# Performance work log

Measured on AMD Instinct MI355X. Metric: run time of the kernel, lower is better.

## Reference

```python
import jax, jax.numpy as jnp
import numpy as np

MODEL_DIM = 1024
NUM_HEADS = 16
HEAD_DIM = MODEL_DIM // NUM_HEADS
B, T = 4, 2048


def setup_inputs() -> dict:
    key = jax.random.key(0)
    ks = jax.random.split(key, 11)
    s = 1.0 / np.sqrt(MODEL_DIM)  # torch Linear default-ish init scale
    def lin(kw, kb):
        W = jax.random.uniform(kw, (MODEL_DIM, MODEL_DIM), jnp.float32, -s, s)
        b = jax.random.uniform(kb, (MODEL_DIM,), jnp.float32, -s, s)
        return W, b
    Wq, bq = lin(ks[0], ks[1])
    Wk, bk = lin(ks[2], ks[3])
    Wv, bv = lin(ks[4], ks[5])
    Wo, bo = lin(ks[6], ks[7])
    query = jax.random.normal(ks[8], (B, T, MODEL_DIM), jnp.float32)
    key_t = jax.random.normal(ks[9], (B, T, MODEL_DIM), jnp.float32)
    value = jax.random.normal(ks[10], (B, T, MODEL_DIM), jnp.float32)
    return {"query": query, "key": key_t, "value": value,
            "Wq": Wq, "bq": bq, "Wk": Wk, "bk": bk,
            "Wv": Wv, "bv": bv, "Wo": Wo, "bo": bo}


def reference(query, key, value, Wq, bq, Wk, bk, Wv, bv, Wo, bo):
    b, tq, d = query.shape
    tk = key.shape[-2]
    h, hd = NUM_HEADS, HEAD_DIM
    # projections; split last dim into heads (torch split/cat == reshape to [b,t,h,hd])
    q = (query @ Wq.T + bq).reshape(b, tq, h, hd)
    k = (key @ Wk.T + bk).reshape(b, tk, h, hd)
    v = (value @ Wv.T + bv).reshape(b, tk, h, hd)
    score = jnp.einsum('bqhd,bkhd->bhqk', q, k) / np.sqrt(hd).astype(np.float32)
    causal = jnp.tril(jnp.ones((tq, tk), dtype=bool))  # mask=True path
    score = jnp.where(causal, score, -jnp.inf)
    probs = jax.nn.softmax(score, axis=-1)
    out = jnp.einsum('bhqk,bkhd->bqhd', probs, v).reshape(b, tq, d)
    return out @ Wo.T + bo
```

## Files before the change

kernel.cpp:

```cpp
#include <hip/hip_runtime.h>
#include <stdint.h>

#define T_SEQ 2048
#define NB    4
#define NH    16
#define DH    64
#define DM    1024
#define MTOT  (NB * T_SEQ)

typedef __attribute__((ext_vector_type(8)))  short  short8;
typedef __attribute__((ext_vector_type(8)))  __bf16 bf16x8;
typedef __attribute__((ext_vector_type(4)))  float  f32x4;
typedef __attribute__((ext_vector_type(16))) float  f32x16;
typedef __attribute__((ext_vector_type(4)))  unsigned short ushort4v;
typedef __attribute__((ext_vector_type(4)))  unsigned int   uint4v;
typedef unsigned short ushort;
typedef unsigned long long u64;

__device__ __forceinline__ ushort f2bf(float x) {
    unsigned int u = __builtin_bit_cast(unsigned int, x);
    u += 0x7FFFu + ((u >> 16) & 1u);
    return (ushort)(u >> 16);
}

__device__ __forceinline__ unsigned cvtpk(float lo, float hi) {
    unsigned r;
    asm("v_cvt_pk_bf16_f32 %0, %1, %2" : "=v"(r) : "v"(lo), "v"(hi));
    return r;
}

__device__ __forceinline__ f32x4 mfma16(short8 a, short8 b, f32x4 c) {
    return __builtin_amdgcn_mfma_f32_16x16x32_bf16(
        __builtin_bit_cast(bf16x8, a), __builtin_bit_cast(bf16x8, b), c, 0, 0, 0);
}
__device__ __forceinline__ f32x16 mfma32(short8 a, short8 b, f32x16 c) {
    return __builtin_amdgcn_mfma_f32_32x32x16_bf16(
        __builtin_bit_cast(bf16x8, a), __builtin_bit_cast(bf16x8, b), c, 0, 0, 0);
}

#define GLOBAL_AS(p) ((const __attribute__((address_space(1))) void*)(p))
#define LDS_AS(p)    ((__attribute__((address_space(3))) void*)(p))

__global__ void cvt4_kernel(const float* __restrict__ s0, const float* __restrict__ s1,
                            const float* __restrict__ s2, const float* __restrict__ s3,
                            ushort* __restrict__ dst) {
    int i = blockIdx.x * 256 + threadIdx.x;
    int which = i >> 18;
    int loc   = i & 262143;
    const float* s = which == 0 ? s0 : which == 1 ? s1 : which == 2 ? s2 : s3;
    f32x4 v = ((const f32x4*)s)[loc];
    ushort4v r;
    r[0] = f2bf(v[0]); r[1] = f2bf(v[1]); r[2] = f2bf(v[2]); r[3] = f2bf(v[3]);
    ((ushort4v*)dst)[i] = r;
}

template <int MODE>
__global__ __launch_bounds__(256, 2)
void gemm_kernel(const void* __restrict__ Xv, const ushort* __restrict__ Wb,
                 const float* __restrict__ bias, void* __restrict__ outv, float scale)
{
    __shared__ __align__(16) ushort sA[128 * 64];
    __shared__ __align__(16) ushort sB[128 * 64];

    const int tid  = threadIdx.x;
    const int lane = tid & 63;
    const int w    = tid >> 6;
    const int wr   = (w >> 1) * 64;
    const int wc   = (w & 1) * 64;
    const int bm   = (blockIdx.x & 63) * 128;
    const int bn   = (blockIdx.x >> 6) * 128;
    const int lr   = lane & 15;
    const int lk   = lane >> 4;

    f32x4 acc[4][4] = {};

    for (int kt = 0; kt < DM; kt += 64) {
        __syncthreads();
        if constexpr (MODE == 0 || MODE == 2) {
            const float* X = (const float*)Xv;
            #pragma unroll
            for (int i = 0; i < 4; ++i) {
                int ofs  = i * 4096 + w * 1024 + lane * 16;
                int row  = ofs >> 7;
                int colB = ofs & 127;
                const float* src = X + (size_t)(bm + row) * DM + kt + (colB >> 1);
                f32x4 v0 = *(const f32x4*)(src);
                f32x4 v1 = *(const f32x4*)(src + 4);
                short8 pk;
                pk[0] = (short)f2bf(v0[0]); pk[1] = (short)f2bf(v0[1]);
                pk[2] = (short)f2bf(v0[2]); pk[3] = (short)f2bf(v0[3]);
                pk[4] = (short)f2bf(v1[0]); pk[5] = (short)f2bf(v1[1]);
                pk[6] = (short)f2bf(v1[2]); pk[7] = (short)f2bf(v1[3]);
                *(short8*)((char*)sA + row * 128 + (colB ^ ((row & 7) << 4))) = pk;
            }
        } else {
            const ushort* X = (const ushort*)Xv;
            #pragma unroll
            for (int i = 0; i < 4; ++i) {
                int ofs  = i * 4096 + w * 1024 + lane * 16;
                int row  = ofs >> 7;
                int colB = (ofs & 127) ^ ((row & 7) << 4);
                const char* src = (const char*)X + ((size_t)(bm + row) * DM + kt) * 2 + colB;
                char* dst = (char*)sA + i * 4096 + w * 1024;
                __builtin_amdgcn_global_load_lds(GLOBAL_AS(src), LDS_AS(dst), 16, 0, 0);
            }
        }
        #pragma unroll
        for (int i = 0; i < 4; ++i) {
            int ofs  = i * 4096 + w * 1024 + lane * 16;
            int row  = ofs >> 7;
            int colB = (ofs & 127) ^ ((row & 7) << 4);
            const char* src = (const char*)Wb + ((size_t)(bn + row) * DM + kt) * 2 + colB;
            char* dst = (char*)sB + i * 4096 + w * 1024;
            __builtin_amdgcn_global_load_lds(GLOBAL_AS(src), LDS_AS(dst), 16, 0, 0);
        }
        __syncthreads();

        #pragma unroll
        for (int kk = 0; kk < 2; ++kk) {
            short8 af[4], bfr[4];
            #pragma unroll
            for (int m = 0; m < 4; ++m) {
                int row = wr + m * 16 + lr;
                int cB  = (kk * 64 + lk * 16) ^ ((row & 7) << 4);
                af[m] = *(const short8*)((const char*)sA + row * 128 + cB);
            }
            #pragma unroll
            for (int n = 0; n < 4; ++n) {
                int row = wc + n * 16 + lr;
                int cB  = (kk * 64 + lk * 16) ^ ((row & 7) << 4);
                bfr[n] = *(const short8*)((const char*)sB + row * 128 + cB);
            }
            #pragma unroll
            for (int m = 0; m < 4; ++m)
                #pragma unroll
                for (int n = 0; n < 4; ++n)
                    acc[m][n] = mfma16(af[m], bfr[n], acc[m][n]);
        }
    }

    #pragma unroll
    for (int m = 0; m < 4; ++m) {
        #pragma unroll
        for (int n = 0; n < 4; ++n) {
            int col   = bn + wc + n * 16 + lr;
            float bv  = bias[col];
            if constexpr (MODE == 2) {
                int row0 = bm + wr + m * 16 + lk * 4;
                int b = row0 >> 11, t0 = row0 & (T_SEQ - 1);
                int h = col >> 6,  d = col & 63;
                int t0p = (t0 & ~12) | ((t0 & 4) << 1) | ((t0 & 8) >> 1);
                u64 pk = 0;
                #pragma unroll
                for (int j = 0; j < 4; ++j)
                    pk |= (u64)f2bf(acc[m][n][j] + bv) << (16 * j);
                *(u64*)((ushort*)outv + ((size_t)((b * NH + h) * DH + d)) * T_SEQ + t0p) = pk;
            } else {
                #pragma unroll
                for (int j = 0; j < 4; ++j) {
                    int row   = bm + wr + m * 16 + lk * 4 + j;
                    float val = (acc[m][n][j] + bv) * scale;
                    if constexpr (MODE == 0) {
                        int b = row >> 11, t = row & (T_SEQ - 1);
                        int h = col >> 6,  d = col & 63;
                        ((ushort*)outv)[((size_t)((b * NH + h) * T_SEQ + t)) * DH + d] = f2bf(val);
                    } else {
                        ((float*)outv)[(size_t)row * DM + col] = val;
                    }
                }
            }
        }
    }
}

__global__ __launch_bounds__(256)
void attn_kernel(const ushort* __restrict__ Q, const ushort* __restrict__ K,
                 const ushort* __restrict__ Vt, ushort* __restrict__ O)
{
    __shared__ __align__(16) ushort sK[2][64 * 64];
    __shared__ __align__(16) ushort sV[2][64 * 64];

    const int tid  = threadIdx.x;
    const int lane = tid & 63;
    const int w    = tid >> 6;
    const int l31  = lane & 31;
    const int hi   = lane >> 5;
    const int bh   = blockIdx.x & 63;
    const int qt   = 15 - (blockIdx.x >> 6);
    const int b    = bh >> 4, h = bh & 15;

    const ushort* Qbh = Q + (size_t)bh * T_SEQ * DH;
    const char*   Kc  = (const char*)(K  + (size_t)bh * T_SEQ * DH);
    const char*   Vc  = (const char*)(Vt + (size_t)bh * DH * T_SEQ);

    const int q0w   = qt * 128 + w * 32;
    const int kvmax = 2 * qt + 1;

    const int scolB = (tid & 7) * 16;

    auto STAGE = [&](int kv, int buf) {
        #pragma unroll
        for (int i = 0; i < 2; ++i) {
            int row = i * 32 + (tid >> 3);
            int cB  = scolB ^ ((row & 7) << 4);
            __builtin_amdgcn_global_load_lds(
                GLOBAL_AS(Kc + (size_t)(kv * 64 + row) * 128 + cB),
                LDS_AS((char*)&sK[buf][0] + i * 4096 + tid * 16), 16, 0, 0);
        }
        #pragma unroll
        for (int i = 0; i < 2; ++i) {
            int row = i * 32 + (tid >> 3);
            int cB  = scolB ^ ((row & 7) << 4);
            __builtin_amdgcn_global_load_lds(
                GLOBAL_AS(Vc + (size_t)row * (T_SEQ * 2) + kv * 128 + cB),
                LDS_AS((char*)&sV[buf][0] + i * 4096 + tid * 16), 16, 0, 0);
        }
    };

    short8 qf[4];
    #pragma unroll
    for (int dc = 0; dc < 4; ++dc)
        qf[dc] = *(const short8*)(Qbh + (size_t)(q0w + l31) * DH + dc * 16 + hi * 8);

    f32x16 o0 = {}, o1 = {};
    float mrow = -1e30f, lsum = 0.f;

    STAGE(0, 0);

    for (int kv = 0; kv <= kvmax; ++kv) {
        const int cur = kv & 1;
        __syncthreads();
        if (kv < kvmax) STAGE(kv + 1, cur ^ 1);
        if (kv * 64 > q0w + 31) continue;

        const char* sk = (const char*)&sK[cur][0];
        const char* sv = (const char*)&sV[cur][0];

        f32x16 s0 = {}, s1 = {};
        __builtin_amdgcn_s_setprio(1);
        #pragma unroll
        for (int dc = 0; dc < 4; ++dc) {
            int cB  = dc * 32 + hi * 16;
            int swz = (l31 & 7) << 4;
            short8 kf0 = *(const short8*)(sk + l31 * 128 + (cB ^ swz));
            short8 kf1 = *(const short8*)(sk + (32 + l31) * 128 + (cB ^ swz));
            s0 = mfma32(kf0, qf[dc], s0);
            s1 = mfma32(kf1, qf[dc], s1);
        }
        __builtin_amdgcn_s_setprio(0);

        if (kv * 64 + 63 > q0w) {
            int q = q0w + l31;
            #pragma unroll
            for (int r = 0; r < 16; ++r) {
                int kp = kv * 64 + (r & 3) + 8 * (r >> 2) + 4 * hi;
                if (kp > q)      s0[r] = -1e30f;
                if (kp + 32 > q) s1[r] = -1e30f;
            }
        }

        float t16[16];
        #pragma unroll
        for (int r = 0; r < 16; ++r) t16[r] = fmaxf(s0[r], s1[r]);
        #pragma unroll
        for (int r = 0; r < 8; ++r)  t16[r] = fmaxf(t16[r], t16[r + 8]);
        #pragma unroll
        for (int r = 0; r < 4; ++r)  t16[r] = fmaxf(t16[r], t16[r + 4]);
        float pm = fmaxf(fmaxf(t16[0], t16[1]), fmaxf(t16[2], t16[3]));
        pm = fmaxf(pm, __shfl_xor(pm, 32));

        if (__any(pm > mrow + 8.f)) {
            float mn = fmaxf(mrow, pm);
            float al = __builtin_amdgcn_exp2f(mrow - mn);
            mrow = mn;
            lsum *= al;
            #pragma unroll
            for (int r = 0; r < 16; ++r) {
                float aq = __shfl(al, (r & 3) + 8 * (r >> 2) + 4 * hi);
                o0[r] *= aq;
                o1[r] *= aq;
            }
        }

        float rs = 0.f;
        #pragma unroll
        for (int r = 0; r < 16; ++r) { s0[r] = __builtin_amdgcn_exp2f(s0[r] - mrow); rs += s0[r]; }
        #pragma unroll
        for (int r = 0; r < 16; ++r) { s1[r] = __builtin_amdgcn_exp2f(s1[r] - mrow); rs += s1[r]; }
        lsum += rs;

        short8 pa[4];
        #pragma unroll
        for (int seg = 0; seg < 4; ++seg) {
            const f32x16& sp = (seg < 2) ? s0 : s1;
            const int r0 = (seg & 1) * 8;
            uint4v pw;
            pw[0] = cvtpk(sp[r0 + 0], sp[r0 + 1]);
            pw[1] = cvtpk(sp[r0 + 2], sp[r0 + 3]);
            pw[2] = cvtpk(sp[r0 + 4], sp[r0 + 5]);
            pw[3] = cvtpk(sp[r0 + 6], sp[r0 + 7]);
            pa[seg] = __builtin_bit_cast(short8, pw);
        }

        __builtin_amdgcn_s_setprio(1);
        #pragma unroll
        for (int seg = 0; seg < 4; ++seg) {
            int cB = seg * 32 + hi * 16;
            {
                int d = l31;
                short8 vf = *(const short8*)(sv + d * 128 + (cB ^ ((d & 7) << 4)));
                o0 = mfma32(pa[seg], vf, o0);
            }
            {
                int d = 32 + l31;
                short8 vf = *(const short8*)(sv + d * 128 + (cB ^ ((d & 7) << 4)));
                o1 = mfma32(pa[seg], vf, o1);
            }
        }
        __builtin_amdgcn_s_setprio(0);
    }

    lsum += __shfl_xor(lsum, 32);
    float rl = 1.0f / lsum;
    #pragma unroll
    for (int r = 0; r < 16; ++r) {
        int   ql = (r & 3) + 8 * (r >> 2) + 4 * hi;
        float rq = __shfl(rl, ql);
        int   t  = q0w + ql;
        size_t base = ((size_t)(b * T_SEQ) + t) * DM + h * DH;
        O[base + l31]      = f2bf(o0[r] * rq);
        O[base + 32 + l31] = f2bf(o1[r] * rq);
    }
}

extern "C" void kernel_launch(void* const* d_in, const int* in_sizes, int n_in,
                              void* d_out, int out_size, void* d_ws, size_t ws_size,
                              hipStream_t stream)
{
    const float* query = (const float*)d_in[0];
    const float* key_t = (const float*)d_in[1];
    const float* value = (const float*)d_in[2];
    const float* Wq = (const float*)d_in[3];
    const float* bq = (const float*)d_in[4];
    const float* Wk = (const float*)d_in[5];
    const float* bk = (const float*)d_in[6];
    const float* Wv = (const float*)d_in[7];
    const float* bv = (const float*)d_in[8];
    const float* Wo = (const float*)d_in[9];
    const float* bo = (const float*)d_in[10];
    float* out = (float*)d_out;

    char* ws = (char*)d_ws;
    const size_t WSZ = (size_t)DM * DM * 2;
    const size_t PSZ = (size_t)MTOT * DM * 2;
    ushort* Wq_b = (ushort*)(ws);
    ushort* Wk_b = (ushort*)(ws + WSZ);
    ushort* Wv_b = (ushort*)(ws + 2 * WSZ);
    ushort* Wo_b = (ushort*)(ws + 3 * WSZ);
    ushort* Qp   = (ushort*)(ws + 4 * WSZ);
    ushort* Kp   = (ushort*)(ws + 4 * WSZ + PSZ);
    ushort* Vt   = (ushort*)(ws + 4 * WSZ + 2 * PSZ);
    ushort* AO   = (ushort*)(ws + 4 * WSZ + 3 * PSZ);

    cvt4_kernel<<<4096, 256, 0, stream>>>(Wq, Wk, Wv, Wo, Wq_b);

    gemm_kernel<0><<<512, 256, 0, stream>>>(query, Wq_b, bq, Qp, 0.18033688011112042f);
    gemm_kernel<0><<<512, 256, 0, stream>>>(key_t, Wk_b, bk, Kp, 1.0f);
    gemm_kernel<2><<<512, 256, 0, stream>>>(value, Wv_b, bv, Vt, 1.0f);

    attn_kernel<<<64 * 16, 256, 0, stream>>>(Qp, Kp, Vt, AO);

    gemm_kernel<1><<<512, 256, 0, stream>>>(AO, Wo_b, bo, out, 1.0f);
}
```

Baseline: 183.2 us.

## Merge QKV projections, double-buffer GEMMs, pair causal tiles in attention

```diff
diff --git a/kernel.cpp b/kernel.cpp
--- a/kernel.cpp
+++ b/kernel.cpp
@@ -54,13 +54,148 @@
     ((ushort4v*)dst)[i] = r;
 }
 
-template <int MODE>
 __global__ __launch_bounds__(256, 2)
-void gemm_kernel(const void* __restrict__ Xv, const ushort* __restrict__ Wb,
-                 const float* __restrict__ bias, void* __restrict__ outv, float scale)
+void proj_gemm(const float* __restrict__ Xq, const float* __restrict__ Xk,
+               const float* __restrict__ Xv, const ushort* __restrict__ Wall,
+               const float* __restrict__ bq, const float* __restrict__ bk,
+               const float* __restrict__ bv, ushort* __restrict__ P0,
+               ushort* __restrict__ Vt, float qscale)
 {
-    __shared__ __align__(16) ushort sA[128 * 64];
-    __shared__ __align__(16) ushort sB[128 * 64];
+    __shared__ __align__(16) ushort sA[2][128 * 64];
+    __shared__ __align__(16) ushort sB[2][128 * 64];
+
+    const int which = blockIdx.x >> 9;
+    const int inner = blockIdx.x & 511;
+    const float* X     = which == 0 ? Xq : which == 1 ? Xk : Xv;
+    const ushort* Wb   = Wall + (size_t)which * DM * DM;
+    const float* bias  = which == 0 ? bq : which == 1 ? bk : bv;
+
+    const int tid  = threadIdx.x;
+    const int lane = tid & 63;
+    const int w    = tid >> 6;
+    const int wr   = (w >> 1) * 64;
+    const int wc   = (w & 1) * 64;
+    const int bm   = (inner & 63) * 128;
+    const int bn   = (inner >> 6) * 128;
+    const int lr   = lane & 15;
+    const int lk   = lane >> 4;
+
+    const int ofs0 = w * 1024 + lane * 16;
+
+    f32x4 areg[8];
+    auto LOAD_A = [&](int kt) {
+        #pragma unroll
+        for (int i = 0; i < 4; ++i) {
+            int ofs  = i * 4096 + ofs0;
+            int row  = ofs >> 7;
+            int colB = ofs & 127;
+            const float* src = X + (size_t)(bm + row) * DM + kt + (colB >> 1);
+            areg[2 * i]     = *(const f32x4*)(src);
+            areg[2 * i + 1] = *(const f32x4*)(src + 4);
+        }
+    };
+    auto WRITE_A = [&](int buf) {
+        #pragma unroll
+        for (int i = 0; i < 4; ++i) {
+            int ofs  = i * 4096 + ofs0;
+            int row  = ofs >> 7;
+            int colB = ofs & 127;
+            f32x4 v0 = areg[2 * i], v1 = areg[2 * i + 1];
+            bf16x8 pk;
+            pk[0] = (__bf16)v0[0]; pk[1] = (__bf16)v0[1];
+            pk[2] = (__bf16)v0[2]; pk[3] = (__bf16)v0[3];
+            pk[4] = (__bf16)v1[0]; pk[5] = (__bf16)v1[1];
+            pk[6] = (__bf16)v1[2]; pk[7] = (__bf16)v1[3];
+            *(bf16x8*)((char*)&sA[buf][0] + row * 128 + (colB ^ ((row & 7) << 4))) = pk;
+        }
+    };
+    auto STAGE_B = [&](int kt, int buf) {
+        #pragma unroll
+        for (int i = 0; i < 4; ++i) {
+            int ofs  = i * 4096 + ofs0;
+            int row  = ofs >> 7;
+            int colB = (ofs & 127) ^ ((row & 7) << 4);
+            __builtin_amdgcn_global_load_lds(
+                GLOBAL_AS((const char*)Wb + ((size_t)(bn + row) * DM + kt) * 2 + colB),
+                LDS_AS((char*)&sB[buf][0] + i * 4096 + ofs0), 16, 0, 0);
+        }
+    };
+
+    f32x4 acc[4][4] = {};
+
+    LOAD_A(0);
+    STAGE_B(0, 0);
+    WRITE_A(0);
+
+    for (int t = 0; t < 16; ++t) {
+        const int cur = t & 1;
+        __syncthreads();
+        if (t < 15) {
+            LOAD_A((t + 1) * 64);
+            STAGE_B((t + 1) * 64, cur ^ 1);
+        }
+        #pragma unroll
+        for (int kk = 0; kk < 2; ++kk) {
+            short8 af[4], bfr[4];
+            #pragma unroll
+            for (int m = 0; m < 4; ++m) {
+                int row = wr + m * 16 + lr;
+                int cB  = (kk * 64 + lk * 16) ^ ((row & 7) << 4);
+                af[m] = *(const short8*)((const char*)&sA[cur][0] + row * 128 + cB);
+            }
+            #pragma unroll
+            for (int n = 0; n < 4; ++n) {
+                int row = wc + n * 16 + lr;
+                int cB  = (kk * 64 + lk * 16) ^ ((row & 7) << 4);
+                bfr[n] = *(const short8*)((const char*)&sB[cur][0] + row * 128 + cB);
+            }
+            #pragma unroll
+            for (int m = 0; m < 4; ++m)
+                #pragma unroll
+                for (int n = 0; n < 4; ++n)
+                    acc[m][n] = mfma16(af[m], bfr[n], acc[m][n]);
+        }
+        if (t < 15) WRITE_A(cur ^ 1);
+    }
+
+    const float scale = (which == 0) ? qscale : 1.0f;
+    #pragma unroll
+    for (int m = 0; m < 4; ++m) {
+        #pragma unroll
+        for (int n = 0; n < 4; ++n) {
+            int col  = bn + wc + n * 16 + lr;
+            float bv = bias[col];
+            if (which == 2) {
+                int row0 = bm + wr + m * 16 + lk * 4;
+                int b = row0 >> 11, t0 = row0 & (T_SEQ - 1);
+                int h = col >> 6,  d = col & 63;
+                int t0p = (t0 & ~12) | ((t0 & 4) << 1) | ((t0 & 8) >> 1);
+                u64 pk = 0;
+                #pragma unroll
+                for (int j = 0; j < 4; ++j)
+                    pk |= (u64)f2bf(acc[m][n][j] + bv) << (16 * j);
+                *(u64*)(Vt + ((size_t)((b * NH + h) * DH + d)) * T_SEQ + t0p) = pk;
+            } else {
+                ushort* outp = P0 + (size_t)which * MTOT * DM;
+                #pragma unroll
+                for (int j = 0; j < 4; ++j) {
+                    int row   = bm + wr + m * 16 + lk * 4 + j;
+                    float val = (acc[m][n][j] + bv) * scale;
+                    int b = row >> 11, t = row & (T_SEQ - 1);
+                    int h = col >> 6,  d = col & 63;
+                    outp[((size_t)((b * NH + h) * T_SEQ + t)) * DH + d] = f2bf(val);
+                }
+            }
+        }
+    }
+}
+
+__global__ __launch_bounds__(256, 2)
+void out_gemm(const ushort* __restrict__ X, const ushort* __restrict__ Wb,
+              const float* __restrict__ bias, float* __restrict__ out)
+{
+    __shared__ __align__(16) ushort sA[2][128 * 64];
+    __shared__ __align__(16) ushort sB[2][128 * 64];
 
     const int tid  = threadIdx.x;
     const int lane = tid & 63;
@@ -71,51 +206,31 @@
     const int bn   = (blockIdx.x >> 6) * 128;
     const int lr   = lane & 15;
     const int lk   = lane >> 4;
-
-    f32x4 acc[4][4] = {};
-
-    for (int kt = 0; kt < DM; kt += 64) {
-        __syncthreads();
-        if constexpr (MODE == 0 || MODE == 2) {
-            const float* X = (const float*)Xv;
-            #pragma unroll
-            for (int i = 0; i < 4; ++i) {
-                int ofs  = i * 4096 + w * 1024 + lane * 16;
-                int row  = ofs >> 7;
-                int colB = ofs & 127;
-                const float* src = X + (size_t)(bm + row) * DM + kt + (colB >> 1);
-                f32x4 v0 = *(const f32x4*)(src);
-                f32x4 v1 = *(const f32x4*)(src + 4);
-                short8 pk;
-                pk[0] = (short)f2bf(v0[0]); pk[1] = (short)f2bf(v0[1]);
-                pk[2] = (short)f2bf(v0[2]); pk[3] = (short)f2bf(v0[3]);
-                pk[4] = (short)f2bf(v1[0]); pk[5] = (short)f2bf(v1[1]);
-                pk[6] = (short)f2bf(v1[2]); pk[7] = (short)f2bf(v1[3]);
-                *(short8*)((char*)sA + row * 128 + (colB ^ ((row & 7) << 4))) = pk;
-            }
-        } else {
-            const ushort* X = (const ushort*)Xv;
-            #pragma unroll
-            for (int i = 0; i < 4; ++i) {
-                int ofs  = i * 4096 + w * 1024 + lane * 16;
-                int row  = ofs >> 7;
-                int colB = (ofs & 127) ^ ((row & 7) << 4);
-                const char* src = (const char*)X + ((size_t)(bm + row) * DM + kt) * 2 + colB;
-                char* dst = (char*)sA + i * 4096 + w * 1024;
-                __builtin_amdgcn_global_load_lds(GLOBAL_AS(src), LDS_AS(dst), 16, 0, 0);
-            }
-        }
+    const int ofs0 = w * 1024 + lane * 16;
+
+    auto STAGE = [&](const ushort* src0, ushort (*dst)[128 * 64], int kt, int buf) {
         #pragma unroll
         for (int i = 0; i < 4; ++i) {
-            int ofs  = i * 4096 + w * 1024 + lane * 16;
+            int ofs  = i * 4096 + ofs0;
             int row  = ofs >> 7;
             int colB = (ofs & 127) ^ ((row & 7) << 4);
-            const char* src = (const char*)Wb + ((size_t)(bn + row) * DM + kt) * 2 + colB;
-            char* dst = (char*)sB + i * 4096 + w * 1024;
-            __builtin_amdgcn_global_load_lds(GLOBAL_AS(src), LDS_AS(dst), 16, 0, 0);
-        }
+            __builtin_amdgcn_global_load_lds(
+                GLOBAL_AS((const char*)src0 + ((size_t)row * DM + kt) * 2 + colB),
+                LDS_AS((char*)&dst[buf][0] + i * 4096 + ofs0), 16, 0, 0);
+        }
+    };
+
+    f32x4 acc[4][4] = {};
+    STAGE(X + (size_t)bm * DM, sA, 0, 0);
+    STAGE(Wb + (size_t)bn * DM, sB, 0, 0);
+
+    for (int t = 0; t < 16; ++t) {
+        const int cur = t & 1;
         __syncthreads();
-
+        if (t < 15) {
+            STAGE(X + (size_t)bm * DM, sA, (t + 1) * 64, cur ^ 1);
+            STAGE(Wb + (size_t)bn * DM, sB, (t + 1) * 64, cur ^ 1);
+        }
         #pragma unroll
         for (int kk = 0; kk < 2; ++kk) {
             short8 af[4], bfr[4];
@@ -123,13 +238,13 @@
             for (int m = 0; m < 4; ++m) {
                 int row = wr + m * 16 + lr;
                 int cB  = (kk * 64 + lk * 16) ^ ((row & 7) << 4);
-                af[m] = *(const short8*)((const char*)sA + row * 128 + cB);
+                af[m] = *(const short8*)((const char*)&sA[cur][0] + row * 128 + cB);
             }
             #pragma unroll
             for (int n = 0; n < 4; ++n) {
                 int row = wc + n * 16 + lr;
                 int cB  = (kk * 64 + lk * 16) ^ ((row & 7) << 4);
-                bfr[n] = *(const short8*)((const char*)sB + row * 128 + cB);
+                bfr[n] = *(const short8*)((const char*)&sB[cur][0] + row * 128 + cB);
             }
             #pragma unroll
             for (int m = 0; m < 4; ++m)
@@ -143,31 +258,12 @@
     for (int m = 0; m < 4; ++m) {
         #pragma unroll
         for (int n = 0; n < 4; ++n) {
-            int col   = bn + wc + n * 16 + lr;
-            float bv  = bias[col];
-            if constexpr (MODE == 2) {
-                int row0 = bm + wr + m * 16 + lk * 4;
-                int b = row0 >> 11, t0 = row0 & (T_SEQ - 1);
-                int h = col >> 6,  d = col & 63;
-                int t0p = (t0 & ~12) | ((t0 & 4) << 1) | ((t0 & 8) >> 1);
-                u64 pk = 0;
-                #pragma unroll
-                for (int j = 0; j < 4; ++j)
-                    pk |= (u64)f2bf(acc[m][n][j] + bv) << (16 * j);
-                *(u64*)((ushort*)outv + ((size_t)((b * NH + h) * DH + d)) * T_SEQ + t0p) = pk;
-            } else {
-                #pragma unroll
-                for (int j = 0; j < 4; ++j) {
-                    int row   = bm + wr + m * 16 + lk * 4 + j;
-                    float val = (acc[m][n][j] + bv) * scale;
-                    if constexpr (MODE == 0) {
-                        int b = row >> 11, t = row & (T_SEQ - 1);
-                        int h = col >> 6,  d = col & 63;
-                        ((ushort*)outv)[((size_t)((b * NH + h) * T_SEQ + t)) * DH + d] = f2bf(val);
-                    } else {
-                        ((float*)outv)[(size_t)row * DM + col] = val;
-                    }
-                }
+            int col  = bn + wc + n * 16 + lr;
+            float bv = bias[col];
+            #pragma unroll
+            for (int j = 0; j < 4; ++j) {
+                int row = bm + wr + m * 16 + lk * 4 + j;
+                out[(size_t)row * DM + col] = acc[m][n][j] + bv;
             }
         }
     }
@@ -185,23 +281,25 @@
     const int w    = tid >> 6;
     const int l31  = lane & 31;
     const int hi   = lane >> 5;
-    const int bh   = blockIdx.x & 63;
-    const int qt   = 15 - (blockIdx.x >> 6);
-    const int b    = bh >> 4, h = bh & 15;
+
+    const int B   = blockIdx.x;
+    const int xcd = B & 7;
+    const int j   = B >> 3;
+    const int bh  = ((j >> 3) << 3) | xcd;
+    const int p   = j & 7;
+    const int b   = bh >> 4, h = bh & 15;
 
     const ushort* Qbh = Q + (size_t)bh * T_SEQ * DH;
     const char*   Kc  = (const char*)(K  + (size_t)bh * T_SEQ * DH);
     const char*   Vc  = (const char*)(Vt + (size_t)bh * DH * T_SEQ);
 
-    const int q0w   = qt * 128 + w * 32;
-    const int kvmax = 2 * qt + 1;
-
     const int scolB = (tid & 7) * 16;
+    const int srow  = tid >> 3;
 
     auto STAGE = [&](int kv, int buf) {
         #pragma unroll
         for (int i = 0; i < 2; ++i) {
-            int row = i * 32 + (tid >> 3);
+            int row = i * 32 + srow;
             int cB  = scolB ^ ((row & 7) << 4);
             __builtin_amdgcn_global_load_lds(
                 GLOBAL_AS(Kc + (size_t)(kv * 64 + row) * 128 + cB),
@@ -209,7 +307,7 @@
         }
         #pragma unroll
         for (int i = 0; i < 2; ++i) {
-            int row = i * 32 + (tid >> 3);
+            int row = i * 32 + srow;
             int cB  = scolB ^ ((row & 7) << 4);
             __builtin_amdgcn_global_load_lds(
                 GLOBAL_AS(Vc + (size_t)row * (T_SEQ * 2) + kv * 128 + cB),
@@ -217,119 +315,125 @@
         }
     };
 
-    short8 qf[4];
-    #pragma unroll
-    for (int dc = 0; dc < 4; ++dc)
-        qf[dc] = *(const short8*)(Qbh + (size_t)(q0w + l31) * DH + dc * 16 + hi * 8);
-
-    f32x16 o0 = {}, o1 = {};
-    float mrow = -1e30f, lsum = 0.f;
-
-    STAGE(0, 0);
-
-    for (int kv = 0; kv <= kvmax; ++kv) {
-        const int cur = kv & 1;
-        __syncthreads();
-        if (kv < kvmax) STAGE(kv + 1, cur ^ 1);
-        if (kv * 64 > q0w + 31) continue;
-
-        const char* sk = (const char*)&sK[cur][0];
-        const char* sv = (const char*)&sV[cur][0];
-
-        f32x16 s0 = {}, s1 = {};
-        __builtin_amdgcn_s_setprio(1);
-        #pragma unroll
-        for (int dc = 0; dc < 4; ++dc) {
-            int cB  = dc * 32 + hi * 16;
-            int swz = (l31 & 7) << 4;
-            short8 kf0 = *(const short8*)(sk + l31 * 128 + (cB ^ swz));
-            short8 kf1 = *(const short8*)(sk + (32 + l31) * 128 + (cB ^ swz));
-            s0 = mfma32(kf0, qf[dc], s0);
-            s1 = mfma32(kf1, qf[dc], s1);
-        }
-        __builtin_amdgcn_s_setprio(0);
-
-        if (kv * 64 + 63 > q0w) {
-            int q = q0w + l31;
-            #pragma unroll
-            for (int r = 0; r < 16; ++r) {
-                int kp = kv * 64 + (r & 3) + 8 * (r >> 2) + 4 * hi;
-                if (kp > q)      s0[r] = -1e30f;
-                if (kp + 32 > q) s1[r] = -1e30f;
-            }
-        }
-
-        float t16[16];
-        #pragma unroll
-        for (int r = 0; r < 16; ++r) t16[r] = fmaxf(s0[r], s1[r]);
-        #pragma unroll
-        for (int r = 0; r < 8; ++r)  t16[r] = fmaxf(t16[r], t16[r + 8]);
-        #pragma unroll
-        for (int r = 0; r < 4; ++r)  t16[r] = fmaxf(t16[r], t16[r + 4]);
-        float pm = fmaxf(fmaxf(t16[0], t16[1]), fmaxf(t16[2], t16[3]));
-        pm = fmaxf(pm, __shfl_xor(pm, 32));
-
-        if (__any(pm > mrow + 8.f)) {
-            float mn = fmaxf(mrow, pm);
-            float al = __builtin_amdgcn_exp2f(mrow - mn);
-            mrow = mn;
-            lsum *= al;
-            #pragma unroll
-            for (int r = 0; r < 16; ++r) {
-                float aq = __shfl(al, (r & 3) + 8 * (r >> 2) + 4 * hi);
-                o0[r] *= aq;
-                o1[r] *= aq;
-            }
-        }
-
-        float rs = 0.f;
-        #pragma unroll
-        for (int r = 0; r < 16; ++r) { s0[r] = __builtin_amdgcn_exp2f(s0[r] - mrow); rs += s0[r]; }
-        #pragma unroll
-        for (int r = 0; r < 16; ++r) { s1[r] = __builtin_amdgcn_exp2f(s1[r] - mrow); rs += s1[r]; }
-        lsum += rs;
-
-        short8 pa[4];
-        #pragma unroll
-        for (int seg = 0; seg < 4; ++seg) {
-            const f32x16& sp = (seg < 2) ? s0 : s1;
-            const int r0 = (seg & 1) * 8;
-            uint4v pw;
-            pw[0] = cvtpk(sp[r0 + 0], sp[r0 + 1]);
-            pw[1] = cvtpk(sp[r0 + 2], sp[r0 + 3]);
-            pw[2] = cvtpk(sp[r0 + 4], sp[r0 + 5]);
-            pw[3] = cvtpk(sp[r0 + 6], sp[r0 + 7]);
-            pa[seg] = __builtin_bit_cast(short8, pw);
-        }
-
-        __builtin_amdgcn_s_setprio(1);
-        #pragma unroll
-        for (int seg = 0; seg < 4; ++seg) {
-            int cB = seg * 32 + hi * 16;
-            {
-                int d = l31;
-                short8 vf = *(const short8*)(sv + d * 128 + (cB ^ ((d & 7) << 4)));
-                o0 = mfma32(pa[seg], vf, o0);
-            }
-            {
-                int d = 32 + l31;
-                short8 vf = *(const short8*)(sv + d * 128 + (cB ^ ((d & 7) << 4)));
-                o1 = mfma32(pa[seg], vf, o1);
-            }
-        }
-        __builtin_amdgcn_s_setprio(0);
-    }
-
-    lsum += __shfl_xor(lsum, 32);
-    float rl = 1.0f / lsum;
-    #pragma unroll
-    for (int r = 0; r < 16; ++r) {
-        int   ql = (r & 3) + 8 * (r >> 2) + 4 * hi;
-        float rq = __shfl(rl, ql);
-        int   t  = q0w + ql;
-        size_t base = ((size_t)(b * T_SEQ) + t) * DM + h * DH;
-        O[base + l31]      = f2bf(o0[r] * rq);
-        O[base + 32 + l31] = f2bf(o1[r] * rq);
+    for (int half = 0; half < 2; ++half) {
+        const int qt    = half == 0 ? 15 - p : p;
+        const int q0w   = qt * 128 + w * 32;
+        const int kvmax = 2 * qt + 1;
+
+        short8 qf[4];
+        #pragma unroll
+        for (int dc = 0; dc < 4; ++dc)
+            qf[dc] = *(const short8*)(Qbh + (size_t)(q0w + l31) * DH + dc * 16 + hi * 8);
+
+        f32x16 o0 = {}, o1 = {};
+        float mrow = -1e30f, lsum = 0.f;
+
+        STAGE(0, 0);
+
+        for (int kv = 0; kv <= kvmax; ++kv) {
+            const int cur = kv & 1;
+            __syncthreads();
+            if (kv < kvmax) STAGE(kv + 1, cur ^ 1);
+            if (kv * 64 > q0w + 31) continue;
+
+            const char* sk = (const char*)&sK[cur][0];
+            const char* sv = (const char*)&sV[cur][0];
+
+            f32x16 s0 = {}, s1 = {};
+            __builtin_amdgcn_s_setprio(1);
+            #pragma unroll
+            for (int dc = 0; dc < 4; ++dc) {
+                int cB  = dc * 32 + hi * 16;
+                int swz = (l31 & 7) << 4;
+                short8 kf0 = *(const short8*)(sk + l31 * 128 + (cB ^ swz));
+                short8 kf1 = *(const short8*)(sk + (32 + l31) * 128 + (cB ^ swz));
+                s0 = mfma32(kf0, qf[dc], s0);
+                s1 = mfma32(kf1, qf[dc], s1);
+            }
+            __builtin_amdgcn_s_setprio(0);
+
+            if (kv * 64 + 63 > q0w) {
+                int q = q0w + l31;
+                #pragma unroll
+                for (int r = 0; r < 16; ++r) {
+                    int kp = kv * 64 + (r & 3) + 8 * (r >> 2) + 4 * hi;
+                    if (kp > q)      s0[r] = -1e30f;
+                    if (kp + 32 > q) s1[r] = -1e30f;
+                }
+            }
+
+            float t16[16];
+            #pragma unroll
+            for (int r = 0; r < 16; ++r) t16[r] = fmaxf(s0[r], s1[r]);
+            #pragma unroll
+            for (int r = 0; r < 8; ++r)  t16[r] = fmaxf(t16[r], t16[r + 8]);
+            #pragma unroll
+            for (int r = 0; r < 4; ++r)  t16[r] = fmaxf(t16[r], t16[r + 4]);
+            float pm = fmaxf(fmaxf(t16[0], t16[1]), fmaxf(t16[2], t16[3]));
+            pm = fmaxf(pm, __shfl_xor(pm, 32));
+
+            if (__any(pm > mrow + 8.f)) {
+                float mn = fmaxf(mrow, pm);
+                float al = __builtin_amdgcn_exp2f(mrow - mn);
+                mrow = mn;
+                lsum *= al;
+                #pragma unroll
+                for (int r = 0; r < 16; ++r) {
+                    float aq = __shfl(al, (r & 3) + 8 * (r >> 2) + 4 * hi);
+                    o0[r] *= aq;
+                    o1[r] *= aq;
+                }
+            }
+
+            float rs = 0.f;
+            #pragma unroll
+            for (int r = 0; r < 16; ++r) { s0[r] = __builtin_amdgcn_exp2f(s0[r] - mrow); rs += s0[r]; }
+            #pragma unroll
+            for (int r = 0; r < 16; ++r) { s1[r] = __builtin_amdgcn_exp2f(s1[r] - mrow); rs += s1[r]; }
+            lsum += rs;
+
+            short8 pa[4];
+            #pragma unroll
+            for (int seg = 0; seg < 4; ++seg) {
+                const f32x16& sp = (seg < 2) ? s0 : s1;
+                const int r0 = (seg & 1) * 8;
+                uint4v pw;
+                pw[0] = cvtpk(sp[r0 + 0], sp[r0 + 1]);
+                pw[1] = cvtpk(sp[r0 + 2], sp[r0 + 3]);
+                pw[2] = cvtpk(sp[r0 + 4], sp[r0 + 5]);
+                pw[3] = cvtpk(sp[r0 + 6], sp[r0 + 7]);
+                pa[seg] = __builtin_bit_cast(short8, pw);
+            }
+
+            __builtin_amdgcn_s_setprio(1);
+            #pragma unroll
+            for (int seg = 0; seg < 4; ++seg) {
+                int cB = seg * 32 + hi * 16;
+                {
+                    int d = l31;
+                    short8 vf = *(const short8*)(sv + d * 128 + (cB ^ ((d & 7) << 4)));
+                    o0 = mfma32(pa[seg], vf, o0);
+                }
+                {
+                    int d = 32 + l31;
+                    short8 vf = *(const short8*)(sv + d * 128 + (cB ^ ((d & 7) << 4)));
+                    o1 = mfma32(pa[seg], vf, o1);
+                }
+            }
+            __builtin_amdgcn_s_setprio(0);
+        }
+
+        lsum += __shfl_xor(lsum, 32);
+        float rl = 1.0f / lsum;
+        #pragma unroll
+        for (int r = 0; r < 16; ++r) {
+            int   ql = (r & 3) + 8 * (r >> 2) + 4 * hi;
+            float rq = __shfl(rl, ql);
+            int   t  = q0w + ql;
+            size_t base = ((size_t)(b * T_SEQ) + t) * DM + h * DH;
+            O[base + l31]      = f2bf(o0[r] * rq);
+            O[base + 32 + l31] = f2bf(o1[r] * rq);
+        }
     }
 }
 
@@ -353,22 +457,19 @@
     char* ws = (char*)d_ws;
     const size_t WSZ = (size_t)DM * DM * 2;
     const size_t PSZ = (size_t)MTOT * DM * 2;
-    ushort* Wq_b = (ushort*)(ws);
-    ushort* Wk_b = (ushort*)(ws + WSZ);
-    ushort* Wv_b = (ushort*)(ws + 2 * WSZ);
+    ushort* Wall = (ushort*)(ws);
     ushort* Wo_b = (ushort*)(ws + 3 * WSZ);
     ushort* Qp   = (ushort*)(ws + 4 * WSZ);
     ushort* Kp   = (ushort*)(ws + 4 * WSZ + PSZ);
     ushort* Vt   = (ushort*)(ws + 4 * WSZ + 2 * PSZ);
     ushort* AO   = (ushort*)(ws + 4 * WSZ + 3 * PSZ);
 
-    cvt4_kernel<<<4096, 256, 0, stream>>>(Wq, Wk, Wv, Wo, Wq_b);
-
-    gemm_kernel<0><<<512, 256, 0, stream>>>(query, Wq_b, bq, Qp, 0.18033688011112042f);
-    gemm_kernel<0><<<512, 256, 0, stream>>>(key_t, Wk_b, bk, Kp, 1.0f);
-    gemm_kernel<2><<<512, 256, 0, stream>>>(value, Wv_b, bv, Vt, 1.0f);
-
-    attn_kernel<<<64 * 16, 256, 0, stream>>>(Qp, Kp, Vt, AO);
-
-    gemm_kernel<1><<<512, 256, 0, stream>>>(AO, Wo_b, bo, out, 1.0f);
-}
+    cvt4_kernel<<<4096, 256, 0, stream>>>(Wq, Wk, Wv, Wo, Wall);
+
+    proj_gemm<<<1536, 256, 0, stream>>>(query, key_t, value, Wall, bq, bk, bv,
+                                        Qp, Vt, 0.18033688011112042f);
+
+    attn_kernel<<<512, 256, 0, stream>>>(Qp, Kp, Vt, AO);
+
+    out_gemm<<<512, 256, 0, stream>>>(AO, Wo_b, bo, out);
+}
```

After: 197.6 us. 7.8% more time.
